# Kernel tuning notes

Measured on AMD Instinct MI355X. Metric: run time of the kernel, lower is better.

## Reference

```python
import jax, jax.numpy as jnp
import numpy as np
from jax import lax

B, CODELEN, COMLEN, NAST, SUBG = 32, 50, 30, 300, 4
EMB, H, ASTHOPS = 300, 256, 2
AST_VOCAB, COM_VOCAB = 10000, 10000


def gru(x, h0, wih, whh, bih, bhh):
    # PyTorch GRU cell semantics. x: [N, T, D], h0: [N, H] -> (ys [N,T,H], hT [N,H])
    xg = jnp.einsum('ntd,gd->ntg', x, wih) + bih  # precompute input gates [N,T,3H]
    def step(h, xt):
        hg = h @ whh.T + bhh
        xr, xz, xn = jnp.split(xt, 3, axis=-1)
        hr, hz, hn = jnp.split(hg, 3, axis=-1)
        r = jax.nn.sigmoid(xr + hr)
        z = jax.nn.sigmoid(xz + hz)
        n = jnp.tanh(xn + r * hn)
        hnew = (1.0 - z) * n + z * h
        return hnew, hnew
    hT, ys = lax.scan(step, h0, jnp.swapaxes(xg, 0, 1))
    return jnp.swapaxes(ys, 0, 1), hT


def dot_attn(q, k):
    # DotProductAttention in eval mode (dropout = identity)
    scale = 1.0 / jnp.sqrt(jnp.asarray(q.shape[-1], q.dtype))
    s = jnp.einsum('bqd,bkd->bqk', q, k) * scale
    return jnp.einsum('bqk,bkd->bqd', jax.nn.softmax(s, axis=-1), k)


def setup_inputs() -> dict:
    key = jax.random.key(0)
    ks = jax.random.split(key, 32)
    def rn(k, shp, sc=0.05):
        return jax.random.normal(k, shp, jnp.float32) * sc
    inp = {}
    inp['x0'] = jax.random.randint(ks[0], (B, CODELEN), 0, AST_VOCAB)
    inp['x1'] = jax.random.randint(ks[1], (B, COMLEN), 0, COM_VOCAB)
    inp['x2'] = jax.random.randint(ks[2], (B, SUBG, NAST), 0, AST_VOCAB)
    inp['adj'] = jax.random.uniform(ks[3], (B, SUBG, NAST, NAST), jnp.float32) * (1.0 / NAST)
    inp['emb_ast'] = rn(ks[4], (AST_VOCAB, EMB), 0.5)
    inp['emb_com'] = rn(ks[5], (COM_VOCAB, EMB), 0.5)
    inp['gru1_wih'] = rn(ks[6], (3 * H, EMB)); inp['gru1_whh'] = rn(ks[7], (3 * H, H))
    inp['gru1_bih'] = rn(ks[8], (3 * H,));    inp['gru1_bhh'] = rn(ks[9], (3 * H,))
    inp['gru2_wih'] = rn(ks[10], (3 * H, EMB)); inp['gru2_whh'] = rn(ks[11], (3 * H, H))
    inp['gru2_bih'] = rn(ks[12], (3 * H,));     inp['gru2_bhh'] = rn(ks[13], (3 * H,))
    inp['gru4_wih'] = rn(ks[14], (3 * H, NAST * EMB), 0.01)
    inp['gru4_whh'] = rn(ks[15], (3 * H, H))
    inp['gru4_bih'] = rn(ks[16], (3 * H,)); inp['gru4_bhh'] = rn(ks[17], (3 * H,))
    inp['gru58_wih'] = rn(ks[18], (SUBG, 3 * H, EMB)); inp['gru58_whh'] = rn(ks[19], (SUBG, 3 * H, H))
    inp['gru58_bih'] = rn(ks[20], (SUBG, 3 * H));      inp['gru58_bhh'] = rn(ks[21], (SUBG, 3 * H))
    inp['gcn_w'] = rn(ks[22], (EMB, EMB)); inp['gcn_b'] = rn(ks[23], (EMB,))
    inp['dense_w'] = rn(ks[24], (H, 3 * H)); inp['dense_b'] = rn(ks[25], (H,))
    inp['lin_w'] = rn(ks[26], (COM_VOCAB, COMLEN * H), 0.01); inp['lin_b'] = rn(ks[27], (COM_VOCAB,))
    return inp


def reference(x0, x1, x2, adj, emb_ast, emb_com,
              gru1_wih, gru1_whh, gru1_bih, gru1_bhh,
              gru2_wih, gru2_whh, gru2_bih, gru2_bhh,
              gru4_wih, gru4_whh, gru4_bih, gru4_bhh,
              gru58_wih, gru58_whh, gru58_bih, gru58_bhh,
              gcn_w, gcn_b, dense_w, dense_b, lin_w, lin_b):
    b = x0.shape[0]
    scale = 1.0 / jnp.sqrt(jnp.float32(H))
    # token encoder + comment decoder
    tencout, tstate = gru(emb_ast[x0], jnp.zeros((b, H), jnp.float32),
                          gru1_wih, gru1_whh, gru1_bih, gru1_bhh)
    decout, _ = gru(emb_com[x1], tstate, gru2_wih, gru2_whh, gru2_bih, gru2_bhh)
    tcontext = dot_attn(decout, tencout)
    # GCN over 4 sub-graphs (torch code mutates astwork in place -> tmp alias sees post-GCN feats)
    astwork = jnp.transpose(emb_ast[x2], (1, 0, 2, 3))  # [4,B,N,300]
    adjp = jnp.transpose(adj, (1, 0, 2, 3))             # [4,B,N,N]
    for _ in range(ASTHOPS):
        support = jnp.einsum('sbnd,de->sbne', astwork, gcn_w)
        astwork = jax.nn.relu(jnp.einsum('sbnm,sbme->sbne', adjp, support) + gcn_b)
    # TimeDistributed(gru4): batch = 4 sub-graphs, sequence = B, input = flattened node feats
    g4in = astwork.reshape(SUBG, b, NAST * EMB)
    g4out, _ = gru(g4in, jnp.zeros((SUBG, H), jnp.float32),
                   gru4_wih, gru4_whh, gru4_bih, gru4_bhh)
    astw = jnp.transpose(g4out, (1, 0, 2))  # [B,4,H]
    ahier = jax.nn.softmax(jnp.einsum('bqd,bsd->bqs', decout, astw) * scale, axis=-1)
    ahier_p = jnp.transpose(ahier, (2, 0, 1))  # [4,B,Q]
    # per-sub-graph node GRUs (gru5..gru8) vmapped over the sub-graph axis
    outs, _ = jax.vmap(gru, in_axes=(0, None, 0, 0, 0, 0))(
        astwork, tstate, gru58_wih, gru58_whh, gru58_bih, gru58_bhh)  # [4,B,N,H]
    sc = jax.nn.softmax(jnp.einsum('bqd,sbkd->sbqk', decout, outs) * scale, axis=-1)
    new_atten = sc * ahier_p[:, :, :, None]  # element_wise_mul with hierarchy weights
    acontext = jnp.einsum('sbqk,sbkd->bqd', new_atten, outs)  # bmm then sum over sub-graphs
    acontext = dot_attn(decout, acontext)
    context = jnp.concatenate([tcontext, decout, acontext], axis=-1)  # [B,Q,768]
    out = jax.nn.relu(context @ dense_w.T + dense_b)
    out = out.reshape(b, -1)  # [B, 7680]
    return out @ lin_w.T + lin_b  # [B, comvocab]
```

## Files before the change

### kernel.cpp

```cpp
#include <hip/hip_runtime.h>
#include <hip/hip_fp16.h>
#include <hip/hip_bf16.h>


typedef __attribute__((ext_vector_type(8))) short  bf16x8;
typedef __attribute__((ext_vector_type(4))) float  f32x4;

__device__ inline unsigned short f2bs(float f) {
  __hip_bfloat16 h = __float2bfloat16(f);
  unsigned short u; __builtin_memcpy(&u, &h, 2); return u;
}

template <bool ABF, bool BBF, int OUTM, bool RELU>
__global__ __launch_bounds__(256) void k_mfma(
    const void* __restrict__ Av, long lda, long a_ss, long a_sb,
    const void* __restrict__ Bv, long ldb, long b_ss, long b_sb,
    void* __restrict__ Cv, long ldc, long c_ss, long c_sb,
    const float* __restrict__ bias, long bias_ss,
    int M, int N, int K, int zb, int ksplit)
{
  __shared__ unsigned short As[128][40];
  __shared__ unsigned short Bs[128][40];
  const int tid = threadIdx.x;
  const int zi = blockIdx.z;
  const int bi = zi / ksplit;
  const int ks = zi - bi * ksplit;
  const int sIdx = bi / zb;
  const int bIdx = bi - sIdx * zb;
  const int row0 = blockIdx.y * 128;
  const int col0 = blockIdx.x * 128;
  const int Kc = ((K + ksplit * 32 - 1) / (ksplit * 32)) * 32;
  const int kbeg = ks * Kc;
  const int kend = min(K, kbeg + Kc);
  if (kbeg >= kend) return;

  const char* Ab = (const char*)Av + ((long)sIdx * a_ss + (long)bIdx * a_sb) * (ABF ? 2 : 4);
  const char* Bb = (const char*)Bv + ((long)sIdx * b_ss + (long)bIdx * b_sb) * (BBF ? 2 : 4);
  char* Cb = (char*)Cv + ((long)sIdx * c_ss + (long)bIdx * c_sb) * ((OUTM == 1 || OUTM == 3) ? 2 : 4);

  const int w = tid >> 6, l = tid & 63;
  const int wr = w >> 1, wc = w & 1;
  const int lr = l & 15, lg = l >> 4;

  f32x4 acc[4][4];
#pragma unroll
  for (int m = 0; m < 4; ++m)
#pragma unroll
    for (int n = 0; n < 4; ++n) acc[m][n] = f32x4{0.f, 0.f, 0.f, 0.f};

  const int sr = tid >> 1;
  const int sk = (tid & 1) * 16;

  for (int kt = kbeg; kt < kend; kt += 32) {
    {
      const int gr = row0 + sr;
      if (ABF) {
        const unsigned short* src = (const unsigned short*)(Ab + ((long)gr * lda + kt + sk) * 2);
        if (gr < M && kt + sk + 16 <= kend) {
          const uint2* p = (const uint2*)src;
          *(uint2*)&As[sr][sk + 0]  = p[0];
          *(uint2*)&As[sr][sk + 4]  = p[1];
          *(uint2*)&As[sr][sk + 8]  = p[2];
          *(uint2*)&As[sr][sk + 12] = p[3];
        } else {
#pragma unroll
          for (int i = 0; i < 16; ++i) {
            const int kk = kt + sk + i;
            As[sr][sk + i] = (gr < M && kk < kend) ? src[i] : (unsigned short)0;
          }
        }
      } else {
        const float* src = (const float*)(Ab + ((long)gr * lda + kt + sk) * 4);
        if (gr < M && kt + sk + 16 <= kend) {
#pragma unroll
          for (int q = 0; q < 4; ++q) {
            const float4 v = ((const float4*)src)[q];
            *(unsigned*)&As[sr][sk + q * 4 + 0] = (unsigned)f2bs(v.x) | ((unsigned)f2bs(v.y) << 16);
            *(unsigned*)&As[sr][sk + q * 4 + 2] = (unsigned)f2bs(v.z) | ((unsigned)f2bs(v.w) << 16);
          }
        } else {
#pragma unroll
          for (int i = 0; i < 16; ++i) {
            const int kk = kt + sk + i;
            As[sr][sk + i] = (gr < M && kk < kend) ? f2bs(src[i]) : (unsigned short)0;
          }
        }
      }
    }
    {
      const int gc = col0 + sr;
      if (BBF) {
        const unsigned short* src = (const unsigned short*)(Bb + ((long)gc * ldb + kt + sk) * 2);
        if (gc < N && kt + sk + 16 <= kend) {
          const uint2* p = (const uint2*)src;
          *(uint2*)&Bs[sr][sk + 0]  = p[0];
          *(uint2*)&Bs[sr][sk + 4]  = p[1];
          *(uint2*)&Bs[sr][sk + 8]  = p[2];
          *(uint2*)&Bs[sr][sk + 12] = p[3];
        } else {
#pragma unroll
          for (int i = 0; i < 16; ++i) {
            const int kk = kt + sk + i;
            Bs[sr][sk + i] = (gc < N && kk < kend) ? src[i] : (unsigned short)0;
          }
        }
      } else {
        const float* src = (const float*)(Bb + ((long)gc * ldb + kt + sk) * 4);
        if (gc < N && kt + sk + 16 <= kend) {
#pragma unroll
          for (int q = 0; q < 4; ++q) {
            const float4 v = ((const float4*)src)[q];
            *(unsigned*)&Bs[sr][sk + q * 4 + 0] = (unsigned)f2bs(v.x) | ((unsigned)f2bs(v.y) << 16);
            *(unsigned*)&Bs[sr][sk + q * 4 + 2] = (unsigned)f2bs(v.z) | ((unsigned)f2bs(v.w) << 16);
          }
        } else {
#pragma unroll
          for (int i = 0; i < 16; ++i) {
            const int kk = kt + sk + i;
            Bs[sr][sk + i] = (gc < N && kk < kend) ? f2bs(src[i]) : (unsigned short)0;
          }
        }
      }
    }
    __syncthreads();
    bf16x8 af[4], bf[4];
#pragma unroll
    for (int m = 0; m < 4; ++m)
      af[m] = *(const bf16x8*)&As[wr * 64 + m * 16 + lr][lg * 8];
#pragma unroll
    for (int n = 0; n < 4; ++n)
      bf[n] = *(const bf16x8*)&Bs[wc * 64 + n * 16 + lr][lg * 8];
#pragma unroll
    for (int m = 0; m < 4; ++m)
#pragma unroll
      for (int n = 0; n < 4; ++n)
        acc[m][n] = __builtin_amdgcn_mfma_f32_16x16x32_bf16(af[m], bf[n], acc[m][n], 0, 0, 0);
    __syncthreads();
  }

  const float* bp = bias ? bias + (long)sIdx * bias_ss : nullptr;
#pragma unroll
  for (int m = 0; m < 4; ++m) {
#pragma unroll
    for (int n = 0; n < 4; ++n) {
      const int col = col0 + wc * 64 + n * 16 + lr;
      const int rb  = row0 + wr * 64 + m * 16 + lg * 4;
      const f32x4 v = acc[m][n];
      if (col >= N) continue;
      if (OUTM == 3) {
        unsigned short* ct = (unsigned short*)Cb + (long)col * ldc + rb;
        if (rb + 4 <= M) {
          ushort4 pk;
          pk.x = f2bs(v[0]); pk.y = f2bs(v[1]); pk.z = f2bs(v[2]); pk.w = f2bs(v[3]);
          *(ushort4*)ct = pk;
        } else {
#pragma unroll
          for (int r = 0; r < 4; ++r) if (rb + r < M) ct[r] = f2bs(v[r]);
        }
      } else {
        const float bv = bp ? bp[col] : 0.f;
#pragma unroll
        for (int r = 0; r < 4; ++r) {
          const int row = rb + r;
          if (row >= M) continue;
          float x = v[r] + bv;
          if (RELU) x = fmaxf(x, 0.f);
          if (OUTM == 0) ((float*)Cb)[(long)row * ldc + col] = x;
          else if (OUTM == 1) ((unsigned short*)Cb)[(long)row * ldc + col] = f2bs(x);
          else atomicAdd((float*)Cb + (long)row * ldc + col, x);
        }
      }
    }
  }
}

template <bool BT, bool RELU, bool GATHER, bool ATOMIC>
__global__ __launch_bounds__(256) void k_gemm(
    const float* __restrict__ A, long lda, long a_ss, long a_sb,
    const float* __restrict__ B, long ldb, long b_ss, long b_sb,
    float* __restrict__ C, long ldc, long c_ss, long c_sb,
    const float* __restrict__ bias, long bias_ss,
    const int* __restrict__ gidx,
    int M, int N, int K, int zb, int ksplit)
{
  __shared__ float As[16][68];
  __shared__ float Bs[16][68];
  const int tid = threadIdx.x;
  const int zi = blockIdx.z;
  const int bi = zi / ksplit;
  const int ks = zi - bi * ksplit;
  const int sIdx = bi / zb;
  const int bIdx = bi - sIdx * zb;
  const int row0 = blockIdx.y * 64;
  const int col0 = blockIdx.x * 64;
  const int Kc = (K + ksplit - 1) / ksplit;
  const int kbeg = ks * Kc;
  const int kend = min(K, kbeg + Kc);

  const float* Ab = A + (long)sIdx * a_ss + (long)bIdx * a_sb;
  const float* Bb = B + (long)sIdx * b_ss + (long)bIdx * b_sb;
  float* Cb = C + (long)sIdx * c_ss + (long)bIdx * c_sb;

  const int tx = tid & 15, ty = tid >> 4;
  float acc[4][4];
#pragma unroll
  for (int i = 0; i < 4; ++i)
#pragma unroll
    for (int j = 0; j < 4; ++j) acc[i][j] = 0.f;

  const int ar = tid >> 2;
  const int ac = (tid & 3) * 4;
  const int am = row0 + ar;
  const bool amok = am < M;
  const float* arow;
  if (GATHER) arow = A + (amok ? (long)gidx[am] * lda : 0);
  else        arow = Ab + (long)am * lda;

  for (int kt = kbeg; kt < kend; kt += 16) {
#pragma unroll
    for (int j = 0; j < 4; ++j) {
      const int kk = kt + ac + j;
      As[ac + j][ar] = (amok && kk < kend) ? arow[kk] : 0.f;
    }
    if (BT) {
      const int br = tid >> 2;
      const int bc = (tid & 3) * 4;
      const int nn = col0 + br;
      const bool bok = nn < N;
      const float* brow = Bb + (long)nn * ldb;
#pragma unroll
      for (int j = 0; j < 4; ++j) {
        const int kk = kt + bc + j;
        Bs[bc + j][br] = (bok && kk < kend) ? brow[kk] : 0.f;
      }
    } else {
      const int br = tid >> 4;
      const int bc = (tid & 15) * 4;
      const int kk = kt + br;
      const float* brow = Bb + (long)kk * ldb;
#pragma unroll
      for (int j = 0; j < 4; ++j) {
        const int nn = col0 + bc + j;
        Bs[br][bc + j] = (kk < kend && nn < N) ? brow[nn] : 0.f;
      }
    }
    __syncthreads();
#pragma unroll
    for (int kk = 0; kk < 16; ++kk) {
      const float4 av = *(const float4*)&As[kk][ty * 4];
      const float4 bv = *(const float4*)&Bs[kk][tx * 4];
      const float aa[4] = {av.x, av.y, av.z, av.w};
      const float bb[4] = {bv.x, bv.y, bv.z, bv.w};
#pragma unroll
      for (int i = 0; i < 4; ++i)
#pragma unroll
        for (int j = 0; j < 4; ++j)
          acc[i][j] = fmaf(aa[i], bb[j], acc[i][j]);
    }
    __syncthreads();
  }

  const float* biasp = bias ? bias + (long)sIdx * bias_ss : nullptr;
#pragma unroll
  for (int i = 0; i < 4; ++i) {
    const int m = row0 + ty * 4 + i;
    if (m >= M) continue;
    float* crow = Cb + (long)m * ldc;
#pragma unroll
    for (int j = 0; j < 4; ++j) {
      const int n = col0 + tx * 4 + j;
      if (n >= N) continue;
      if (ATOMIC) {
        atomicAdd(&crow[n], acc[i][j]);
      } else {
        float v = acc[i][j];
        if (biasp) v += biasp[n];
        if (RELU) v = fmaxf(v, 0.f);
        crow[n] = v;
      }
    }
  }
}

__global__ __launch_bounds__(256) void k_init_bias(
    float* __restrict__ C, const float* __restrict__ bias, int M, int N)
{
  const int total = M * N;
  for (int i = blockIdx.x * 256 + threadIdx.x; i < total; i += gridDim.x * 256)
    C[i] = bias[i % N];
}

__global__ __launch_bounds__(256) void k_gather_ast(
    const float* __restrict__ emb, const int* __restrict__ x2,
    unsigned short* __restrict__ outp)
{
  const int total = 4 * 32 * 300 * 300;
  for (int idx = blockIdx.x * 256 + threadIdx.x; idx < total; idx += gridDim.x * 256) {
    const int d = idx % 300;
    const int r = idx / 300;
    const int n = r % 300;
    const int r2 = r / 300;
    const int b = r2 % 32;
    const int s = r2 / 32;
    outp[idx] = f2bs(emb[(long)x2[(b * 4 + s) * 300 + n] * 300 + d]);
  }
}

__global__ __launch_bounds__(256) void k_twb(
    const float* __restrict__ w, unsigned short* __restrict__ o, int R, int C)
{
  const int total = R * C;
  for (int i = blockIdx.x * 256 + threadIdx.x; i < total; i += gridDim.x * 256) {
    const int r = i / C, c = i - r * C;
    o[(long)c * R + r] = f2bs(w[i]);
  }
}

__global__ __launch_bounds__(256) void k_f2b(
    const float* __restrict__ a, unsigned short* __restrict__ o, int n)
{
  for (int i = blockIdx.x * 256 + threadIdx.x; i < n; i += gridDim.x * 256)
    o[i] = f2bs(a[i]);
}

__global__ __launch_bounds__(512) void k_gru_seq(
    const float* __restrict__ xg,
    const float* __restrict__ h0, int h0_mod,
    const float* __restrict__ whh, long w_stride, int cpw,
    const float* __restrict__ bhh, long b_stride,
    float* __restrict__ ys, float* __restrict__ hT, int T)
{
  const int c = blockIdx.x;
  const int tid = threadIdx.x;
  const int j = tid >> 1;
  const int kh = tid & 1;
  const int w = c / cpw;
  const float* W = whh + (long)w * w_stride;
  const float* Bh = bhh + (long)w * b_stride;

  __half2 wr[64], wz[64], wn[64];
  {
    const float* pr = W + (long)j * 256 + kh * 128;
    const float* pz = W + (long)(j + 256) * 256 + kh * 128;
    const float* pn = W + (long)(j + 512) * 256 + kh * 128;
#pragma unroll
    for (int i = 0; i < 64; ++i) {
      wr[i] = __floats2half2_rn(pr[2 * i], pr[2 * i + 1]);
      wz[i] = __floats2half2_rn(pz[2 * i], pz[2 * i + 1]);
      wn[i] = __floats2half2_rn(pn[2 * i], pn[2 * i + 1]);
    }
  }
  const float br = Bh[j], bz = Bh[256 + j], bn = Bh[512 + j];

  __shared__ float  h32[2][256];
  __shared__ __half h16[2][256];
  if (kh == 0) {
    const float hv = h0 ? h0[(long)(c % h0_mod) * 256 + j] : 0.f;
    h32[0][j] = hv;
    h16[0][j] = __float2half(hv);
  }
  __syncthreads();

  const float* xrow = xg + (long)c * T * 768;
  float* yrow = ys ? ys + (long)c * T * 256 : nullptr;
  float xr = 0.f, xz = 0.f, xn = 0.f;
  if (kh == 0) { xr = xrow[j]; xz = xrow[256 + j]; xn = xrow[512 + j]; }
  int cur = 0;
  for (int t = 0; t < T; ++t) {
    float nxr = 0.f, nxz = 0.f, nxn = 0.f;
    if (kh == 0 && t + 1 < T) {
      const float* nx = xrow + (long)(t + 1) * 768;
      nxr = nx[j]; nxz = nx[256 + j]; nxn = nx[512 + j];
    }
    const __half2* hp = (const __half2*)&h16[cur][kh * 128];
    float sr = 0.f, sz = 0.f, sn = 0.f;
#pragma unroll
    for (int i0 = 0; i0 < 64; i0 += 8) {
      __half2 ar = __float2half2_rn(0.f);
      __half2 az = __float2half2_rn(0.f);
      __half2 an = __float2half2_rn(0.f);
#pragma unroll
      for (int i = 0; i < 8; ++i) {
        const __half2 hv = hp[i0 + i];
        ar = __hfma2(wr[i0 + i], hv, ar);
        az = __hfma2(wz[i0 + i], hv, az);
        an = __hfma2(wn[i0 + i], hv, an);
      }
      sr += __low2float(ar) + __high2float(ar);
      sz += __low2float(az) + __high2float(az);
      sn += __low2float(an) + __high2float(an);
    }
    sr += __shfl_xor(sr, 1);
    sz += __shfl_xor(sz, 1);
    sn += __shfl_xor(sn, 1);
    if (kh == 0) {
      const float rr = 1.f / (1.f + __expf(-(xr + sr + br)));
      const float zg = 1.f / (1.f + __expf(-(xz + sz + bz)));
      const float narg = xn + rr * (sn + bn);
      const float e = __expf(-2.f * fabsf(narg));
      const float nv = copysignf((1.f - e) / (1.f + e), narg);
      const float hnew = (1.f - zg) * nv + zg * h32[cur][j];
      h32[cur ^ 1][j] = hnew;
      h16[cur ^ 1][j] = __float2half(hnew);
      if (yrow) yrow[(long)t * 256 + j] = hnew;
    }
    __syncthreads();
    cur ^= 1;
    xr = nxr; xz = nxz; xn = nxn;
  }
  if (hT && kh == 0) hT[(long)c * 256 + j] = h32[cur][j];
}

__global__ __launch_bounds__(256) void k_attn(
    const float* __restrict__ q, const float* __restrict__ kv,
    float* __restrict__ out, int Q, int L)
{
  const int bq = blockIdx.x;
  const int b = bq / Q;
  const int tid = threadIdx.x;
  const int g = tid >> 3, l = tid & 7;
  __shared__ float qv[256];
  __shared__ float sc[64];
  qv[tid] = q[(long)bq * 256 + tid];
  __syncthreads();
  for (int k0 = 0; k0 < L; k0 += 32) {
    const int k = k0 + g;
    float s = 0.f;
    if (k < L) {
      const float* kr = kv + ((long)b * L + k) * 256;
      for (int d = l; d < 256; d += 8) s += qv[d] * kr[d];
    }
    s += __shfl_xor(s, 1);
    s += __shfl_xor(s, 2);
    s += __shfl_xor(s, 4);
    if (k < L && l == 0) sc[k] = s * 0.0625f;
  }
  __syncthreads();
  float m = -1e30f;
  for (int k = 0; k < L; ++k) m = fmaxf(m, sc[k]);
  float den = 0.f;
  for (int k = 0; k < L; ++k) den += __expf(sc[k] - m);
  __syncthreads();
  if (tid < L) sc[tid] = __expf(sc[tid] - m);
  __syncthreads();
  const float* kb = kv + (long)b * L * 256;
  float acc = 0.f;
  for (int k = 0; k < L; ++k) acc += sc[k] * kb[(long)k * 256 + tid];
  out[(long)bq * 256 + tid] = acc / den;
}

__global__ __launch_bounds__(64) void k_hier(
    const float* __restrict__ dec, const float* __restrict__ g4out,
    float* __restrict__ ahier, int Q)
{
  const int bq = blockIdx.x;
  const int b = bq / Q;
  const int l = threadIdx.x;
  float s[4] = {0.f, 0.f, 0.f, 0.f};
#pragma unroll
  for (int i = 0; i < 4; ++i) {
    const int d = l * 4 + i;
    const float qd = dec[(long)bq * 256 + d];
#pragma unroll
    for (int sg = 0; sg < 4; ++sg)
      s[sg] += qd * g4out[((long)sg * 32 + b) * 256 + d];
  }
#pragma unroll
  for (int off = 32; off >= 1; off >>= 1)
#pragma unroll
    for (int sg = 0; sg < 4; ++sg) s[sg] += __shfl_xor(s[sg], off);
  if (l == 0) {
    float m = -1e30f;
#pragma unroll
    for (int sg = 0; sg < 4; ++sg) m = fmaxf(m, s[sg] * 0.0625f);
    float e[4], den = 0.f;
#pragma unroll
    for (int sg = 0; sg < 4; ++sg) { e[sg] = __expf(s[sg] * 0.0625f - m); den += e[sg]; }
#pragma unroll
    for (int sg = 0; sg < 4; ++sg) ahier[(long)bq * 4 + sg] = e[sg] / den;
  }
}

__global__ __launch_bounds__(64) void k_smax(
    float* __restrict__ sc, const float* __restrict__ ahier)
{
  const int id = blockIdx.x;
  const int s = id / 960;
  const int bq = id - s * 960;
  float* row = sc + (long)id * 300;
  const int l = threadIdx.x;
  float v[5];
  float m = -1e30f;
#pragma unroll
  for (int i = 0; i < 5; ++i) {
    const int k = l + i * 64;
    v[i] = (k < 300) ? row[k] * 0.0625f : -1e30f;
    m = fmaxf(m, v[i]);
  }
#pragma unroll
  for (int off = 32; off >= 1; off >>= 1) m = fmaxf(m, __shfl_xor(m, off));
  float den = 0.f;
#pragma unroll
  for (int i = 0; i < 5; ++i) { v[i] = __expf(v[i] - m); den += v[i]; }
#pragma unroll
  for (int off = 32; off >= 1; off >>= 1) den += __shfl_xor(den, off);
  const float w = ahier[(long)bq * 4 + s] / den;
#pragma unroll
  for (int i = 0; i < 5; ++i) {
    const int k = l + i * 64;
    if (k < 300) row[k] = v[i] * w;
  }
}

__global__ __launch_bounds__(256) void k_concat(
    const float* __restrict__ a, const float* __restrict__ b,
    const float* __restrict__ c, float* __restrict__ out, int rows)
{
  const int total = rows * 768;
  for (int i = blockIdx.x * 256 + threadIdx.x; i < total; i += gridDim.x * 256) {
    const int r = i / 768, col = i - r * 768;
    float v;
    if (col < 256) v = a[(long)r * 256 + col];
    else if (col < 512) v = b[(long)r * 256 + col - 256];
    else v = c[(long)r * 256 + col - 512];
    out[i] = v;
  }
}

extern "C" void kernel_launch(void* const* d_in, const int* in_sizes, int n_in,
                              void* d_out, int out_size, void* d_ws, size_t ws_size,
                              hipStream_t stream) {
  const int*   x0      = (const int*)d_in[0];
  const int*   x1      = (const int*)d_in[1];
  const int*   x2      = (const int*)d_in[2];
  const float* adj     = (const float*)d_in[3];
  const float* emb_ast = (const float*)d_in[4];
  const float* emb_com = (const float*)d_in[5];
  const float* g1_wih  = (const float*)d_in[6];
  const float* g1_whh  = (const float*)d_in[7];
  const float* g1_bih  = (const float*)d_in[8];
  const float* g1_bhh  = (const float*)d_in[9];
  const float* g2_wih  = (const float*)d_in[10];
  const float* g2_whh  = (const float*)d_in[11];
  const float* g2_bih  = (const float*)d_in[12];
  const float* g2_bhh  = (const float*)d_in[13];
  const float* g4_wih  = (const float*)d_in[14];
  const float* g4_whh  = (const float*)d_in[15];
  const float* g4_bih  = (const float*)d_in[16];
  const float* g4_bhh  = (const float*)d_in[17];
  const float* g58_wih = (const float*)d_in[18];
  const float* g58_whh = (const float*)d_in[19];
  const float* g58_bih = (const float*)d_in[20];
  const float* g58_bhh = (const float*)d_in[21];
  const float* gcn_w   = (const float*)d_in[22];
  const float* gcn_b   = (const float*)d_in[23];
  const float* dw      = (const float*)d_in[24];
  const float* db      = (const float*)d_in[25];
  const float* lw      = (const float*)d_in[26];
  const float* lb      = (const float*)d_in[27];
  float* out = (float*)d_out;
  float* ws  = (float*)d_ws;

  unsigned short* astwork_bf = (unsigned short*)ws;
  unsigned short* supportT   = (unsigned short*)(ws + 5760000L);
  float* g58xg   = ws + 11520000L;
  float* outsb   = ws + 41011200L;
  float* xg1     = ws + 50841600L;
  float* tenc    = ws + 52070400L;
  float* tstate  = ws + 52480000L;
  float* xg2     = ws + 52488192L;
  float* dec     = ws + 53225472L;
  float* tctx    = ws + 53471232L;
  float* g4xg    = ws + 53716992L;
  float* g4out   = ws + 53815296L;
  float* ahier   = ws + 53848064L;
  float* actx1   = ws + 53851904L;
  float* actx    = ws + 54097664L;
  float* dense   = ws + 54343424L;
  float* ctmp    = ws + 54589184L;
  float* scbuf   = ws + 55326464L;
  unsigned short* gcn_wT   = (unsigned short*)(ws + 56478464L);
  unsigned short* dense_bf = (unsigned short*)(ws + 56523464L);

  const dim3 blk(256);

  k_gather_ast<<<dim3(4096), blk, 0, stream>>>(emb_ast, x2, astwork_bf);
  k_twb<<<dim3(90), blk, 0, stream>>>(gcn_w, gcn_wT, 300, 300);

  for (int hop = 0; hop < 2; ++hop) {
    k_mfma<true, true, 3, false><<<dim3(3, 3, 128), blk, 0, stream>>>(
        astwork_bf, 300, 2880000, 90000,
        gcn_wT, 300, 0, 0,
        supportT, 300, 2880000, 90000,
        nullptr, 0, 300, 300, 300, 32, 1);
    k_mfma<false, true, 1, true><<<dim3(3, 3, 128), blk, 0, stream>>>(
        adj, 300, 90000, 360000,
        supportT, 300, 2880000, 90000,
        astwork_bf, 300, 2880000, 90000,
        gcn_b, 0, 300, 300, 300, 32, 1);
  }

  k_gemm<true, false, true, false><<<dim3(12, 25, 1), blk, 0, stream>>>(
      emb_ast, 300, 0, 0, g1_wih, 300, 0, 0, xg1, 768, 0, 0,
      g1_bih, 0, x0, 1600, 768, 300, 1, 1);
  k_gru_seq<<<dim3(32), dim3(512), 0, stream>>>(
      xg1, nullptr, 1, g1_whh, 0, 1, g1_bhh, 0, tenc, tstate, 50);

  k_gemm<true, false, true, false><<<dim3(12, 15, 1), blk, 0, stream>>>(
      emb_com, 300, 0, 0, g2_wih, 300, 0, 0, xg2, 768, 0, 0,
      g2_bih, 0, x1, 960, 768, 300, 1, 1);
  k_gru_seq<<<dim3(32), dim3(512), 0, stream>>>(
      xg2, tstate, 32, g2_whh, 0, 1, g2_bhh, 0, dec, nullptr, 30);

  k_attn<<<dim3(960), blk, 0, stream>>>(dec, tenc, tctx, 30, 50);

  k_init_bias<<<dim3(384), blk, 0, stream>>>(g4xg, g4_bih, 128, 768);
  k_mfma<true, false, 2, false><<<dim3(6, 1, 43), blk, 0, stream>>>(
      astwork_bf, 90000, 0, 0, g4_wih, 90000, 0, 0, g4xg, 768, 0, 0,
      nullptr, 0, 128, 768, 90000, 1, 43);
  k_gru_seq<<<dim3(4), dim3(512), 0, stream>>>(
      g4xg, nullptr, 1, g4_whh, 0, 1, g4_bhh, 0, g4out, nullptr, 32);

  k_hier<<<dim3(960), dim3(64), 0, stream>>>(dec, g4out, ahier, 30);

  k_mfma<true, false, 0, false><<<dim3(6, 75, 4), blk, 0, stream>>>(
      astwork_bf, 300, 2880000, 0, g58_wih, 300, 230400, 0,
      g58xg, 768, 7372800, 0, g58_bih, 768, 9600, 768, 300, 1, 1);
  k_gru_seq<<<dim3(128), dim3(512), 0, stream>>>(
      g58xg, tstate, 32, g58_whh, 196608, 32, g58_bhh, 768, outsb, nullptr, 300);

  k_gemm<true, false, false, false><<<dim3(5, 1, 128), blk, 0, stream>>>(
      dec, 256, 0, 7680, outsb, 256, 2457600, 76800, scbuf, 300, 288000, 9000,
      nullptr, 0, nullptr, 30, 300, 256, 32, 1);
  k_smax<<<dim3(3840), dim3(64), 0, stream>>>(scbuf, ahier);
  hipMemsetAsync(actx1, 0, 245760 * sizeof(float), stream);
  k_gemm<false, false, false, true><<<dim3(4, 1, 128), blk, 0, stream>>>(
      scbuf, 300, 288000, 9000, outsb, 256, 2457600, 76800, actx1, 256, 0, 7680,
      nullptr, 0, nullptr, 30, 256, 300, 32, 1);

  k_attn<<<dim3(960), blk, 0, stream>>>(dec, actx1, actx, 30, 30);

  k_concat<<<dim3(2880), blk, 0, stream>>>(tctx, dec, actx, ctmp, 960);
  k_gemm<true, true, false, false><<<dim3(4, 15, 1), blk, 0, stream>>>(
      ctmp, 768, 0, 0, dw, 768, 0, 0, dense, 256, 0, 0,
      db, 0, nullptr, 960, 256, 768, 1, 1);
  k_f2b<<<dim3(960), blk, 0, stream>>>(dense, dense_bf, 245760);

  k_init_bias<<<dim3(1250), blk, 0, stream>>>(out, lb, 32, 10000);
  k_mfma<true, false, 2, false><<<dim3(79, 1, 6), blk, 0, stream>>>(
      dense_bf, 7680, 0, 0, lw, 7680, 0, 0, out, 10000, 0, 0,
      nullptr, 0, 32, 10000, 7680, 1, 6);
}
```

Before: 1.819 ms.

## Batch GRU recurrences onto MFMA and move all fp32 GEMMs to MFMA kernel

Replaces the per-sequence GRU kernel (one block per chain, half2 FMA matvec) with a kernel that batches 16 chains per block and computes h·Whh^T with bf16 MFMA, keeping the weights in registers and h in LDS. It also retires the scalar fp32 tiled GEMM and routes the input-gate projections, attention scores/context and dense layer through the MFMA GEMM, adding gather and K-by-N B-layout options. This targets the latency-bound serial recurrence, especially the 300-step sub-graph GRUs, and the slow FP32 FMA GEMMs. The cost is bf16 rounding of the hidden state and weights, plus far fewer blocks per GRU launch.

```diff
diff --git a/kernel.cpp b/kernel.cpp
--- a/kernel.cpp
+++ b/kernel.cpp
@@ -11,12 +11,19 @@
   unsigned short u; __builtin_memcpy(&u, &h, 2); return u;
 }
 
-template <bool ABF, bool BBF, int OUTM, bool RELU>
+__device__ inline float sigf(float x) { return 1.f / (1.f + __expf(-x)); }
+__device__ inline float tanhf_(float x) {
+  const float e = __expf(-2.f * fabsf(x));
+  return copysignf((1.f - e) / (1.f + e), x);
+}
+
+template <bool ABF, bool BBF, int OUTM, bool RELU, bool GATHER = false, bool BKN = false>
 __global__ __launch_bounds__(256) void k_mfma(
     const void* __restrict__ Av, long lda, long a_ss, long a_sb,
     const void* __restrict__ Bv, long ldb, long b_ss, long b_sb,
     void* __restrict__ Cv, long ldc, long c_ss, long c_sb,
     const float* __restrict__ bias, long bias_ss,
+    const int* __restrict__ gidx,
     int M, int N, int K, int zb, int ksplit)
 {
   __shared__ unsigned short As[128][40];
@@ -70,7 +77,9 @@
           }
         }
       } else {
-        const float* src = (const float*)(Ab + ((long)gr * lda + kt + sk) * 4);
+        const float* src;
+        if (GATHER) src = (const float*)Av + ((gr < M) ? (long)gidx[gr] * lda : 0) + kt + sk;
+        else        src = (const float*)(Ab + ((long)gr * lda + kt + sk) * 4);
         if (gr < M && kt + sk + 16 <= kend) {
 #pragma unroll
           for (int q = 0; q < 4; ++q) {
@@ -87,7 +96,30 @@
         }
       }
     }
-    {
+    if (BKN) {
+      const int kk = tid >> 3;
+      const int cb = (tid & 7) * 16;
+      const int gk = kt + kk;
+      const float* brow = (const float*)(Bb + (long)gk * ldb * 4);
+#pragma unroll
+      for (int q = 0; q < 4; ++q) {
+        const int gc = col0 + cb + q * 4;
+        float4 v = float4{0.f, 0.f, 0.f, 0.f};
+        if (gk < kend) {
+          if (gc + 4 <= N) v = *(const float4*)&brow[gc];
+          else {
+            if (gc + 0 < N) v.x = brow[gc + 0];
+            if (gc + 1 < N) v.y = brow[gc + 1];
+            if (gc + 2 < N) v.z = brow[gc + 2];
+            if (gc + 3 < N) v.w = brow[gc + 3];
+          }
+        }
+        Bs[cb + q * 4 + 0][kk] = f2bs(v.x);
+        Bs[cb + q * 4 + 1][kk] = f2bs(v.y);
+        Bs[cb + q * 4 + 2][kk] = f2bs(v.z);
+        Bs[cb + q * 4 + 3][kk] = f2bs(v.w);
+      }
+    } else {
       const int gc = col0 + sr;
       if (BBF) {
         const unsigned short* src = (const unsigned short*)(Bb + ((long)gc * ldb + kt + sk) * 2);
@@ -174,111 +206,150 @@
   }
 }
 
-template <bool BT, bool RELU, bool GATHER, bool ATOMIC>
-__global__ __launch_bounds__(256) void k_gemm(
-    const float* __restrict__ A, long lda, long a_ss, long a_sb,
-    const float* __restrict__ B, long ldb, long b_ss, long b_sb,
-    float* __restrict__ C, long ldc, long c_ss, long c_sb,
-    const float* __restrict__ bias, long bias_ss,
-    const int* __restrict__ gidx,
-    int M, int N, int K, int zb, int ksplit)
-{
-  __shared__ float As[16][68];
-  __shared__ float Bs[16][68];
+__global__ __launch_bounds__(512, 1) void k_gru_mfma(
+    const float* __restrict__ xg,
+    const float* __restrict__ h0, int h0_mod,
+    const float* __restrict__ whh, long w_stride, int cpw,
+    const float* __restrict__ bhh, long b_stride,
+    float* __restrict__ ys, float* __restrict__ hT,
+    int T, int ctot)
+{
+  const int g = blockIdx.x;
   const int tid = threadIdx.x;
-  const int zi = blockIdx.z;
-  const int bi = zi / ksplit;
-  const int ks = zi - bi * ksplit;
-  const int sIdx = bi / zb;
-  const int bIdx = bi - sIdx * zb;
-  const int row0 = blockIdx.y * 64;
-  const int col0 = blockIdx.x * 64;
-  const int Kc = (K + ksplit - 1) / ksplit;
-  const int kbeg = ks * Kc;
-  const int kend = min(K, kbeg + Kc);
-
-  const float* Ab = A + (long)sIdx * a_ss + (long)bIdx * a_sb;
-  const float* Bb = B + (long)sIdx * b_ss + (long)bIdx * b_sb;
-  float* Cb = C + (long)sIdx * c_ss + (long)bIdx * c_sb;
-
-  const int tx = tid & 15, ty = tid >> 4;
-  float acc[4][4];
-#pragma unroll
-  for (int i = 0; i < 4; ++i)
-#pragma unroll
-    for (int j = 0; j < 4; ++j) acc[i][j] = 0.f;
-
-  const int ar = tid >> 2;
-  const int ac = (tid & 3) * 4;
-  const int am = row0 + ar;
-  const bool amok = am < M;
-  const float* arow;
-  if (GATHER) arow = A + (amok ? (long)gidx[am] * lda : 0);
-  else        arow = Ab + (long)am * lda;
-
-  for (int kt = kbeg; kt < kend; kt += 16) {
-#pragma unroll
-    for (int j = 0; j < 4; ++j) {
-      const int kk = kt + ac + j;
-      As[ac + j][ar] = (amok && kk < kend) ? arow[kk] : 0.f;
-    }
-    if (BT) {
-      const int br = tid >> 2;
-      const int bc = (tid & 3) * 4;
-      const int nn = col0 + br;
-      const bool bok = nn < N;
-      const float* brow = Bb + (long)nn * ldb;
-#pragma unroll
-      for (int j = 0; j < 4; ++j) {
-        const int kk = kt + bc + j;
-        Bs[bc + j][br] = (bok && kk < kend) ? brow[kk] : 0.f;
+  const int c0 = g * 16;
+  const int nc = min(16, ctot - c0);
+  const int widx = c0 / cpw;
+  const float* W  = whh + (long)widx * w_stride;
+  const float* Bh = bhh + (long)widx * b_stride;
+
+  const int wv = tid >> 6;
+  const int l  = tid & 63;
+  const int lr = l & 15;
+  const int lg = l >> 4;
+
+  const int chain = tid & 15;
+  const int jb    = tid >> 4;
+  const int j0    = jb * 8;
+  const int c     = c0 + chain;
+  const bool vld  = chain < nc;
+
+  __shared__ unsigned short A_lds[2][8][64][8];
+  __shared__ float gate_lds[16][772];
+  __shared__ float bhh_lds[768];
+
+  for (int i = tid; i < 768; i += 512) bhh_lds[i] = Bh[i];
+
+  bf16x8 bfr[2][3][8];
+#pragma unroll
+  for (int p = 0; p < 2; ++p)
+#pragma unroll
+    for (int nt = 0; nt < 3; ++nt) {
+      const int col = wv * 96 + (p * 3 + nt) * 16 + lr;
+      const float* wp = W + (long)col * 256 + lg * 8;
+#pragma unroll
+      for (int kt = 0; kt < 8; ++kt) {
+        const float4 v0 = *(const float4*)(wp + kt * 32);
+        const float4 v1 = *(const float4*)(wp + kt * 32 + 4);
+        bf16x8 pk;
+        pk[0] = (short)f2bs(v0.x); pk[1] = (short)f2bs(v0.y);
+        pk[2] = (short)f2bs(v0.z); pk[3] = (short)f2bs(v0.w);
+        pk[4] = (short)f2bs(v1.x); pk[5] = (short)f2bs(v1.y);
+        pk[6] = (short)f2bs(v1.z); pk[7] = (short)f2bs(v1.w);
+        bfr[p][nt][kt] = pk;
       }
+    }
+
+  float h[8];
+#pragma unroll
+  for (int e = 0; e < 8; ++e)
+    h[e] = (vld && h0) ? h0[(long)(c % h0_mod) * 256 + j0 + e] : 0.f;
+  {
+    bf16x8 pk;
+#pragma unroll
+    for (int e = 0; e < 8; ++e) pk[e] = (short)f2bs(h[e]);
+    *(bf16x8*)&A_lds[0][jb >> 2][(jb & 3) * 16 + chain][0] = pk;
+  }
+  __syncthreads();
+
+  const float* xrow = xg + (long)c * T * 768 + j0;
+  float* yrow = ys ? ys + (long)c * T * 256 + j0 : nullptr;
+  int cur = 0;
+
+  for (int t = 0; t < T; ++t) {
+    float xr[8], xz[8], xn_[8];
+    if (vld) {
+      const float* xp = xrow + (long)t * 768;
+      *(float4*)&xr[0]  = *(const float4*)(xp);
+      *(float4*)&xr[4]  = *(const float4*)(xp + 4);
+      *(float4*)&xz[0]  = *(const float4*)(xp + 256);
+      *(float4*)&xz[4]  = *(const float4*)(xp + 260);
+      *(float4*)&xn_[0] = *(const float4*)(xp + 512);
+      *(float4*)&xn_[4] = *(const float4*)(xp + 516);
     } else {
-      const int br = tid >> 4;
-      const int bc = (tid & 15) * 4;
-      const int kk = kt + br;
-      const float* brow = Bb + (long)kk * ldb;
-#pragma unroll
-      for (int j = 0; j < 4; ++j) {
-        const int nn = col0 + bc + j;
-        Bs[br][bc + j] = (kk < kend && nn < N) ? brow[nn] : 0.f;
+#pragma unroll
+      for (int e = 0; e < 8; ++e) { xr[e] = 0.f; xz[e] = 0.f; xn_[e] = 0.f; }
+    }
+
+#pragma unroll
+    for (int p = 0; p < 2; ++p) {
+      f32x4 acc[3];
+#pragma unroll
+      for (int nt = 0; nt < 3; ++nt) acc[nt] = f32x4{0.f, 0.f, 0.f, 0.f};
+#pragma unroll
+      for (int kt = 0; kt < 8; ++kt) {
+        const bf16x8 af = *(const bf16x8*)&A_lds[cur][kt][l][0];
+#pragma unroll
+        for (int nt = 0; nt < 3; ++nt)
+          acc[nt] = __builtin_amdgcn_mfma_f32_16x16x32_bf16(af, bfr[p][nt][kt], acc[nt], 0, 0, 0);
       }
+#pragma unroll
+      for (int nt = 0; nt < 3; ++nt) {
+        const int col = wv * 96 + (p * 3 + nt) * 16 + lr;
+#pragma unroll
+        for (int r = 0; r < 4; ++r)
+          gate_lds[lg * 4 + r][col] = acc[nt][r];
+      }
     }
     __syncthreads();
-#pragma unroll
-    for (int kk = 0; kk < 16; ++kk) {
-      const float4 av = *(const float4*)&As[kk][ty * 4];
-      const float4 bv = *(const float4*)&Bs[kk][tx * 4];
-      const float aa[4] = {av.x, av.y, av.z, av.w};
-      const float bb[4] = {bv.x, bv.y, bv.z, bv.w};
-#pragma unroll
-      for (int i = 0; i < 4; ++i)
-#pragma unroll
-        for (int j = 0; j < 4; ++j)
-          acc[i][j] = fmaf(aa[i], bb[j], acc[i][j]);
+
+    float gr[8], gz[8], gn[8], br[8], bz[8], bn[8];
+    *(float4*)&gr[0] = *(const float4*)&gate_lds[chain][j0];
+    *(float4*)&gr[4] = *(const float4*)&gate_lds[chain][j0 + 4];
+    *(float4*)&gz[0] = *(const float4*)&gate_lds[chain][256 + j0];
+    *(float4*)&gz[4] = *(const float4*)&gate_lds[chain][256 + j0 + 4];
+    *(float4*)&gn[0] = *(const float4*)&gate_lds[chain][512 + j0];
+    *(float4*)&gn[4] = *(const float4*)&gate_lds[chain][512 + j0 + 4];
+    *(float4*)&br[0] = *(const float4*)&bhh_lds[j0];
+    *(float4*)&br[4] = *(const float4*)&bhh_lds[j0 + 4];
+    *(float4*)&bz[0] = *(const float4*)&bhh_lds[256 + j0];
+    *(float4*)&bz[4] = *(const float4*)&bhh_lds[256 + j0 + 4];
+    *(float4*)&bn[0] = *(const float4*)&bhh_lds[512 + j0];
+    *(float4*)&bn[4] = *(const float4*)&bhh_lds[512 + j0 + 4];
+#pragma unroll
+    for (int e = 0; e < 8; ++e) {
+      const float rr = sigf(xr[e] + gr[e] + br[e]);
+      const float zz = sigf(xz[e] + gz[e] + bz[e]);
+      const float nv = tanhf_(xn_[e] + rr * (gn[e] + bn[e]));
+      h[e] = (1.f - zz) * nv + zz * h[e];
+    }
+    {
+      bf16x8 pk;
+#pragma unroll
+      for (int e = 0; e < 8; ++e) pk[e] = (short)f2bs(h[e]);
+      *(bf16x8*)&A_lds[cur ^ 1][jb >> 2][(jb & 3) * 16 + chain][0] = pk;
+    }
+    if (vld && yrow) {
+      float* yp = yrow + (long)t * 256;
+      *(float4*)yp = *(const float4*)&h[0];
+      *(float4*)(yp + 4) = *(const float4*)&h[4];
     }
     __syncthreads();
-  }
-
-  const float* biasp = bias ? bias + (long)sIdx * bias_ss : nullptr;
-#pragma unroll
-  for (int i = 0; i < 4; ++i) {
-    const int m = row0 + ty * 4 + i;
-    if (m >= M) continue;
-    float* crow = Cb + (long)m * ldc;
-#pragma unroll
-    for (int j = 0; j < 4; ++j) {
-      const int n = col0 + tx * 4 + j;
-      if (n >= N) continue;
-      if (ATOMIC) {
-        atomicAdd(&crow[n], acc[i][j]);
-      } else {
-        float v = acc[i][j];
-        if (biasp) v += biasp[n];
-        if (RELU) v = fmaxf(v, 0.f);
-        crow[n] = v;
-      }
-    }
+    cur ^= 1;
+  }
+  if (hT && vld) {
+    float* hp = hT + (long)c * 256 + j0;
+    *(float4*)hp = *(const float4*)&h[0];
+    *(float4*)(hp + 4) = *(const float4*)&h[4];
   }
 }
 
@@ -321,94 +392,6 @@
 {
   for (int i = blockIdx.x * 256 + threadIdx.x; i < n; i += gridDim.x * 256)
     o[i] = f2bs(a[i]);
-}
-
-__global__ __launch_bounds__(512) void k_gru_seq(
-    const float* __restrict__ xg,
-    const float* __restrict__ h0, int h0_mod,
-    const float* __restrict__ whh, long w_stride, int cpw,
-    const float* __restrict__ bhh, long b_stride,
-    float* __restrict__ ys, float* __restrict__ hT, int T)
-{
-  const int c = blockIdx.x;
-  const int tid = threadIdx.x;
-  const int j = tid >> 1;
-  const int kh = tid & 1;
-  const int w = c / cpw;
-  const float* W = whh + (long)w * w_stride;
-  const float* Bh = bhh + (long)w * b_stride;
-
-  __half2 wr[64], wz[64], wn[64];
-  {
-    const float* pr = W + (long)j * 256 + kh * 128;
-    const float* pz = W + (long)(j + 256) * 256 + kh * 128;
-    const float* pn = W + (long)(j + 512) * 256 + kh * 128;
-#pragma unroll
-    for (int i = 0; i < 64; ++i) {
-      wr[i] = __floats2half2_rn(pr[2 * i], pr[2 * i + 1]);
-      wz[i] = __floats2half2_rn(pz[2 * i], pz[2 * i + 1]);
-      wn[i] = __floats2half2_rn(pn[2 * i], pn[2 * i + 1]);
-    }
-  }
-  const float br = Bh[j], bz = Bh[256 + j], bn = Bh[512 + j];
-
-  __shared__ float  h32[2][256];
-  __shared__ __half h16[2][256];
-  if (kh == 0) {
-    const float hv = h0 ? h0[(long)(c % h0_mod) * 256 + j] : 0.f;
-    h32[0][j] = hv;
-    h16[0][j] = __float2half(hv);
-  }
-  __syncthreads();
-
-  const float* xrow = xg + (long)c * T * 768;
-  float* yrow = ys ? ys + (long)c * T * 256 : nullptr;
-  float xr = 0.f, xz = 0.f, xn = 0.f;
-  if (kh == 0) { xr = xrow[j]; xz = xrow[256 + j]; xn = xrow[512 + j]; }
-  int cur = 0;
-  for (int t = 0; t < T; ++t) {
-    float nxr = 0.f, nxz = 0.f, nxn = 0.f;
-    if (kh == 0 && t + 1 < T) {
-      const float* nx = xrow + (long)(t + 1) * 768;
-      nxr = nx[j]; nxz = nx[256 + j]; nxn = nx[512 + j];
-    }
-    const __half2* hp = (const __half2*)&h16[cur][kh * 128];
-    float sr = 0.f, sz = 0.f, sn = 0.f;
-#pragma unroll
-    for (int i0 = 0; i0 < 64; i0 += 8) {
-      __half2 ar = __float2half2_rn(0.f);
-      __half2 az = __float2half2_rn(0.f);
-      __half2 an = __float2half2_rn(0.f);
-#pragma unroll
-      for (int i = 0; i < 8; ++i) {
-        const __half2 hv = hp[i0 + i];
-        ar = __hfma2(wr[i0 + i], hv, ar);
-        az = __hfma2(wz[i0 + i], hv, az);
-        an = __hfma2(wn[i0 + i], hv, an);
-      }
-      sr += __low2float(ar) + __high2float(ar);
-      sz += __low2float(az) + __high2float(az);
-      sn += __low2float(an) + __high2float(an);
-    }
-    sr += __shfl_xor(sr, 1);
-    sz += __shfl_xor(sz, 1);
-    sn += __shfl_xor(sn, 1);
-    if (kh == 0) {
-      const float rr = 1.f / (1.f + __expf(-(xr + sr + br)));
-      const float zg = 1.f / (1.f + __expf(-(xz + sz + bz)));
-      const float narg = xn + rr * (sn + bn);
-      const float e = __expf(-2.f * fabsf(narg));
-      const float nv = copysignf((1.f - e) / (1.f + e), narg);
-      const float hnew = (1.f - zg) * nv + zg * h32[cur][j];
-      h32[cur ^ 1][j] = hnew;
-      h16[cur ^ 1][j] = __float2half(hnew);
-      if (yrow) yrow[(long)t * 256 + j] = hnew;
-    }
-    __syncthreads();
-    cur ^= 1;
-    xr = nxr; xz = nxz; xn = nxn;
-  }
-  if (hT && kh == 0) hT[(long)c * 256 + j] = h32[cur][j];
 }
 
 __global__ __launch_bounds__(256) void k_attn(
@@ -592,56 +575,56 @@
         astwork_bf, 300, 2880000, 90000,
         gcn_wT, 300, 0, 0,
         supportT, 300, 2880000, 90000,
-        nullptr, 0, 300, 300, 300, 32, 1);
+        nullptr, 0, nullptr, 300, 300, 300, 32, 1);
     k_mfma<false, true, 1, true><<<dim3(3, 3, 128), blk, 0, stream>>>(
         adj, 300, 90000, 360000,
         supportT, 300, 2880000, 90000,
         astwork_bf, 300, 2880000, 90000,
-        gcn_b, 0, 300, 300, 300, 32, 1);
-  }
-
-  k_gemm<true, false, true, false><<<dim3(12, 25, 1), blk, 0, stream>>>(
+        gcn_b, 0, nullptr, 300, 300, 300, 32, 1);
+  }
+
+  k_mfma<false, false, 0, false, true><<<dim3(6, 13, 1), blk, 0, stream>>>(
       emb_ast, 300, 0, 0, g1_wih, 300, 0, 0, xg1, 768, 0, 0,
       g1_bih, 0, x0, 1600, 768, 300, 1, 1);
-  k_gru_seq<<<dim3(32), dim3(512), 0, stream>>>(
-      xg1, nullptr, 1, g1_whh, 0, 1, g1_bhh, 0, tenc, tstate, 50);
-
-  k_gemm<true, false, true, false><<<dim3(12, 15, 1), blk, 0, stream>>>(
+  k_gru_mfma<<<dim3(2), dim3(512), 0, stream>>>(
+      xg1, nullptr, 1, g1_whh, 0, 32, g1_bhh, 0, tenc, tstate, 50, 32);
+
+  k_mfma<false, false, 0, false, true><<<dim3(6, 8, 1), blk, 0, stream>>>(
       emb_com, 300, 0, 0, g2_wih, 300, 0, 0, xg2, 768, 0, 0,
       g2_bih, 0, x1, 960, 768, 300, 1, 1);
-  k_gru_seq<<<dim3(32), dim3(512), 0, stream>>>(
-      xg2, tstate, 32, g2_whh, 0, 1, g2_bhh, 0, dec, nullptr, 30);
+  k_gru_mfma<<<dim3(2), dim3(512), 0, stream>>>(
+      xg2, tstate, 32, g2_whh, 0, 32, g2_bhh, 0, dec, nullptr, 30, 32);
 
   k_attn<<<dim3(960), blk, 0, stream>>>(dec, tenc, tctx, 30, 50);
 
   k_init_bias<<<dim3(384), blk, 0, stream>>>(g4xg, g4_bih, 128, 768);
   k_mfma<true, false, 2, false><<<dim3(6, 1, 43), blk, 0, stream>>>(
       astwork_bf, 90000, 0, 0, g4_wih, 90000, 0, 0, g4xg, 768, 0, 0,
-      nullptr, 0, 128, 768, 90000, 1, 43);
-  k_gru_seq<<<dim3(4), dim3(512), 0, stream>>>(
-      g4xg, nullptr, 1, g4_whh, 0, 1, g4_bhh, 0, g4out, nullptr, 32);
+      nullptr, 0, nullptr, 128, 768, 90000, 1, 43);
+  k_gru_mfma<<<dim3(1), dim3(512), 0, stream>>>(
+      g4xg, nullptr, 1, g4_whh, 0, 16, g4_bhh, 0, g4out, nullptr, 32, 4);
 
   k_hier<<<dim3(960), dim3(64), 0, stream>>>(dec, g4out, ahier, 30);
 
   k_mfma<true, false, 0, false><<<dim3(6, 75, 4), blk, 0, stream>>>(
       astwork_bf, 300, 2880000, 0, g58_wih, 300, 230400, 0,
-      g58xg, 768, 7372800, 0, g58_bih, 768, 9600, 768, 300, 1, 1);
-  k_gru_seq<<<dim3(128), dim3(512), 0, stream>>>(
-      g58xg, tstate, 32, g58_whh, 196608, 32, g58_bhh, 768, outsb, nullptr, 300);
-
-  k_gemm<true, false, false, false><<<dim3(5, 1, 128), blk, 0, stream>>>(
+      g58xg, 768, 7372800, 0, g58_bih, 768, nullptr, 9600, 768, 300, 1, 1);
+  k_gru_mfma<<<dim3(8), dim3(512), 0, stream>>>(
+      g58xg, tstate, 32, g58_whh, 196608, 32, g58_bhh, 768, outsb, nullptr, 300, 128);
+
+  k_mfma<false, false, 0, false><<<dim3(3, 1, 128), blk, 0, stream>>>(
       dec, 256, 0, 7680, outsb, 256, 2457600, 76800, scbuf, 300, 288000, 9000,
       nullptr, 0, nullptr, 30, 300, 256, 32, 1);
   k_smax<<<dim3(3840), dim3(64), 0, stream>>>(scbuf, ahier);
   hipMemsetAsync(actx1, 0, 245760 * sizeof(float), stream);
-  k_gemm<false, false, false, true><<<dim3(4, 1, 128), blk, 0, stream>>>(
+  k_mfma<false, false, 2, false, false, true><<<dim3(2, 1, 128), blk, 0, stream>>>(
       scbuf, 300, 288000, 9000, outsb, 256, 2457600, 76800, actx1, 256, 0, 7680,
       nullptr, 0, nullptr, 30, 256, 300, 32, 1);
 
   k_attn<<<dim3(960), blk, 0, stream>>>(dec, actx1, actx, 30, 30);
 
   k_concat<<<dim3(2880), blk, 0, stream>>>(tctx, dec, actx, ctmp, 960);
-  k_gemm<true, true, false, false><<<dim3(4, 15, 1), blk, 0, stream>>>(
+  k_mfma<false, false, 0, true><<<dim3(2, 8, 1), blk, 0, stream>>>(
       ctmp, 768, 0, 0, dw, 768, 0, 0, dense, 256, 0, 0,
       db, 0, nullptr, 960, 256, 768, 1, 1);
   k_f2b<<<dim3(960), blk, 0, stream>>>(dense, dense_bf, 245760);
@@ -649,5 +632,5 @@
   k_init_bias<<<dim3(1250), blk, 0, stream>>>(out, lb, 32, 10000);
   k_mfma<true, false, 2, false><<<dim3(79, 1, 6), blk, 0, stream>>>(
       dense_bf, 7680, 0, 0, lw, 7680, 0, 0, out, 10000, 0, 0,
-      nullptr, 0, 32, 10000, 7680, 1, 6);
-}
+      nullptr, 0, nullptr, 32, 10000, 7680, 1, 6);
+}
```

New measurement: 2.911 ms. +60.0%, slower.
